# Optimization experiments

Hardware: AMD Instinct MI355X
Metric: run time of the kernel (lower is better)

Reference implementation:

```python
import jax, jax.numpy as jnp
import numpy as np

TOP_K = 4
NORM_TOPK_PROB = False  # Qwen2-MoE default

def setup_inputs() -> dict:
    key = jax.random.key(0)
    ks = jax.random.split(key, 10)
    B, S, D = 1, 2048, 2048
    E, F, FS = 8, 1408, 5632
    s = 0.02
    return {
        "hidden_states": jax.random.normal(ks[0], (B, S, D), jnp.float32),
        "gate_w": jax.random.normal(ks[1], (E, D), jnp.float32) * s,          # router Linear weight [E, D]
        "Wg": jax.random.normal(ks[2], (E, D, F), jnp.float32) * s,           # expert gate_proj
        "Wu": jax.random.normal(ks[3], (E, D, F), jnp.float32) * s,           # expert up_proj
        "Wd": jax.random.normal(ks[4], (E, F, D), jnp.float32) * s,           # expert down_proj
        "Wsg": jax.random.normal(ks[5], (D, FS), jnp.float32) * s,            # shared gate_proj
        "Wsu": jax.random.normal(ks[6], (D, FS), jnp.float32) * s,            # shared up_proj
        "Wsd": jax.random.normal(ks[7], (FS, D), jnp.float32) * s,            # shared down_proj
        "shared_gate_w": jax.random.normal(ks[8], (D, 1), jnp.float32) * s,   # shared_expert_gate Linear(D,1)
    }

def reference(hidden_states, gate_w, Wg, Wu, Wd, Wsg, Wsu, Wsd, shared_gate_w):
    B, S, D = hidden_states.shape
    x = hidden_states.reshape(-1, D)                       # [T, D]
    T = x.shape[0]
    router_logits = x @ gate_w.T                           # [T, E]
    probs = jax.nn.softmax(router_logits.astype(jnp.float32), axis=-1)
    top_vals, top_idx = jax.lax.top_k(probs, TOP_K)        # [T, K]
    if NORM_TOPK_PROB:
        top_vals = top_vals / jnp.sum(top_vals, axis=-1, keepdims=True)
    # dense routing-weight matrix: zero for unselected experts (same math as masked naive loop)
    w = jnp.zeros_like(probs).at[jnp.arange(T)[:, None], top_idx].set(top_vals)
    w = w.astype(x.dtype)                                  # [T, E]
    # per-expert SiLU-gated MLP, computed densely over all experts
    h = jax.nn.silu(jnp.einsum('td,edf->etf', x, Wg)) * jnp.einsum('td,edf->etf', x, Wu)  # [E, T, F]
    expert_out = jnp.einsum('etf,efd->etd', h, Wd)         # [E, T, D]
    moe_out = jnp.einsum('etd,te->td', expert_out, w)      # [T, D]
    # shared expert with sigmoid gate
    shared = (jax.nn.silu(x @ Wsg) * (x @ Wsu)) @ Wsd      # [T, D]
    shared = jax.nn.sigmoid(x @ shared_gate_w) * shared    # [T,1] * [T,D]
    out = (moe_out + shared).reshape(B, S, D)
    return out, router_logits
```

## Files before the change

kernel.cpp:

```cpp
#include <hip/hip_runtime.h>
#include <hip/hip_bf16.h>

typedef __attribute__((ext_vector_type(8))) __bf16 bf16x8;
typedef __attribute__((ext_vector_type(4))) float f32x4;

#define TKN 2048
#define DMODEL 2048
#define NEXP 8
#define FEXP 1408
#define FSH 5632

__device__ __forceinline__ unsigned short f2bf(float f) {
  unsigned u = __float_as_uint(f);
  u += 0x7FFFu + ((u >> 16) & 1u);
  return (unsigned short)(u >> 16);
}
__device__ __forceinline__ unsigned pk2(float a, float b) {
  return (unsigned)f2bf(a) | ((unsigned)f2bf(b) << 16);
}

__device__ __forceinline__ void gll16(const void* g, void* l) {
  __builtin_amdgcn_global_load_lds(
      (const __attribute__((address_space(1))) unsigned*)g,
      (__attribute__((address_space(3))) unsigned*)l, 16, 0, 0);
}

enum { EPI_GU = 0, EPI_DOWN = 1, EPI_SDOWN = 2 };

__global__ __launch_bounds__(256)
void router_k(const float* __restrict__ x, const float* __restrict__ gw,
              const float* __restrict__ sgw, float* __restrict__ logits,
              float* __restrict__ sig, int* __restrict__ cnt,
              int* __restrict__ tokl, float* __restrict__ wls)
{
  const int wv = threadIdx.x >> 6, lane = threadIdx.x & 63;
  const int t = blockIdx.x * 4 + wv;
  const float* xr = x + (long)t * DMODEL;
  float xv[32];
#pragma unroll
  for (int j = 0; j < 32; j++) xv[j] = xr[lane + (j << 6)];

  float lg[8];
#pragma unroll
  for (int e = 0; e < 8; e++) {
    const float* gr = gw + (long)e * DMODEL;
    float acc = 0.f;
#pragma unroll
    for (int j = 0; j < 32; j++) acc += xv[j] * gr[lane + (j << 6)];
#pragma unroll
    for (int s = 1; s < 64; s <<= 1) acc += __shfl_xor(acc, s, 64);
    lg[e] = acc;
  }
  float sgacc = 0.f;
#pragma unroll
  for (int j = 0; j < 32; j++) sgacc += xv[j] * sgw[lane + (j << 6)];
#pragma unroll
  for (int s = 1; s < 64; s <<= 1) sgacc += __shfl_xor(sgacc, s, 64);

  if (lane == 0) {
    float mx = lg[0];
#pragma unroll
    for (int e = 1; e < 8; e++) mx = fmaxf(mx, lg[e]);
    float p[8], se = 0.f;
#pragma unroll
    for (int e = 0; e < 8; e++) { p[e] = expf(lg[e] - mx); se += p[e]; }
    float inv = 1.f / se;
#pragma unroll
    for (int e = 0; e < 8; e++) { p[e] *= inv; logits[t * 8 + e] = lg[e]; }
    sig[t] = 1.f / (1.f + expf(-sgacc));
#pragma unroll
    for (int k = 0; k < 4; k++) {
      int bi = 0; float bv = p[0];
#pragma unroll
      for (int e = 1; e < 8; e++) if (p[e] > bv) { bv = p[e]; bi = e; }
      p[bi] = -1.f;
      int pos = atomicAdd(&cnt[bi], 1);
      tokl[bi * TKN + pos] = t;
      wls[bi * TKN + pos] = bv;
    }
  }
}

__global__ void scan_k(const int* __restrict__ cnt, int* __restrict__ offs) {
  if (threadIdx.x == 0) {
    int s = 0;
    for (int e = 0; e < 8; e++) { offs[e] = s; s += cnt[e]; }
    offs[8] = s;
  }
}

__global__ __launch_bounds__(256)
void cvt_x_k(const float* __restrict__ x, char* __restrict__ xbf)
{
  long id = (long)blockIdx.x * 256 + threadIdx.x;
  int row = id >> 8, u = id & 255, kt = u >> 2, j = u & 3;
  const float* p = x + (long)row * 2048 + kt * 32 + j * 4;
  float4 a = *(const float4*)p;
  float4 b = *(const float4*)(p + 16);
  uint4 o;
  o.x = pk2(a.x, a.y); o.y = pk2(a.z, a.w);
  o.z = pk2(b.x, b.y); o.w = pk2(b.z, b.w);
  *(uint4*)(xbf + id * 16) = o;
}

__global__ __launch_bounds__(256)
void cvt_w_k(const float* __restrict__ W, long sB, int N,
             char* __restrict__ panel, long panStride)
{
  const int ct = blockIdx.x, kt = blockIdx.y, e = blockIdx.z, KT = gridDim.y;
  const float* Wp = W + (long)e * sB + (long)(kt * 32) * N + ct * 128;
  __shared__ float t[32][128];
  const int r = threadIdx.x >> 3, q = threadIdx.x & 7;
  const float* rp = Wp + (long)r * N + q * 16;
  float4 f0 = *(const float4*)(rp + 0);
  float4 f1 = *(const float4*)(rp + 4);
  float4 f2 = *(const float4*)(rp + 8);
  float4 f3 = *(const float4*)(rp + 12);
  *(float4*)&t[r][q * 16 + 0]  = f0;
  *(float4*)&t[r][q * 16 + 4]  = f1;
  *(float4*)&t[r][q * 16 + 8]  = f2;
  *(float4*)&t[r][q * 16 + 12] = f3;
  __syncthreads();
  char* outp = panel + e * panStride + ((long)ct * KT + kt) * 8192;
#pragma unroll
  for (int uu = 0; uu < 2; uu++) {
    int u = threadIdx.x + uu * 256;
    int c = u >> 2;
    int g = (u & 3) ^ ((c >> 1) & 3);
    uint4 o;
    o.x = pk2(t[g * 4 + 0][c], t[g * 4 + 1][c]);
    o.y = pk2(t[g * 4 + 2][c], t[g * 4 + 3][c]);
    o.z = pk2(t[16 + g * 4 + 0][c], t[16 + g * 4 + 1][c]);
    o.w = pk2(t[16 + g * 4 + 2][c], t[16 + g * 4 + 3][c]);
    *(uint4*)(outp + u * 16) = o;
  }
}

template<int EPI, bool EXPERT, int KSPLIT>
__global__ __launch_bounds__(256, 2)
void gemm2_k(const char* __restrict__ Abf, long strA,
             const char* __restrict__ Bp, const char* __restrict__ Bp2,
             long sBpan, int KTtot, int NCT,
             void* __restrict__ O, int ldKo,
             const int* __restrict__ cnt, const int* __restrict__ offs,
             const int* __restrict__ tokl, const float* __restrict__ wls,
             const float* __restrict__ sig)
{
  constexpr bool FUSED = (EPI == EPI_GU);
  const int tid = threadIdx.x, lane = tid & 63, w = tid >> 6;
  const int wg = blockIdx.x;

  int e = 0, rt, ct, kc = 0, M = TKN;
  if (EXPERT) {
    e = wg & 7; int q = wg >> 3; rt = q & 15; ct = q >> 4;
    M = cnt[e];
    if (rt * 128 >= M) return;
  } else {
    rt = wg & 15; int q = wg >> 4; ct = q % NCT; kc = q / NCT;
  }
  const int KT = KTtot / KSPLIT;
  const int kt0 = kc * KT;
  const int obase = EXPERT ? offs[e] : 0;

  __shared__ int s_tok[128];
  __shared__ float s_w[128];
  __shared__ alignas(16) char Ab[3][8192];
  __shared__ alignas(16) char Bb[3][8192];
  __shared__ alignas(16) char Bb2[FUSED ? 3 : 1][FUSED ? 8192 : 16];

  if (EXPERT) {
    if (tid < 128) {
      int r = rt * 128 + tid;
      int rc = (r < M) ? r : (M - 1);
      s_tok[tid] = tokl[e * TKN + rc];
      if (EPI == EPI_DOWN) s_w[tid] = (r < M) ? wls[e * TKN + r] : 0.f;
    }
    __syncthreads();
  }

  const int lrow0 = w * 32 + (lane >> 2);
  const int lrow1 = lrow0 + 16;
  auto rowbyte = [&](int rl) -> long {
    long gr;
    if (EPI == EPI_DOWN) { int r = rt * 128 + rl; gr = obase + ((r < M) ? r : (M - 1)); }
    else if (EXPERT)     { gr = s_tok[rl]; }
    else                 { gr = rt * 128 + rl; }
    return gr * strA;
  };
  const int au0 = (lane & 3) ^ ((lrow0 >> 1) & 3);
  const int au1 = (lane & 3) ^ ((lrow1 >> 1) & 3);
  const char* gA0 = Abf + rowbyte(lrow0) + (long)kt0 * 64 + au0 * 16;
  const char* gA1 = Abf + rowbyte(lrow1) + (long)kt0 * 64 + au1 * 16;
  const long bbase = (EXPERT ? (long)e * sBpan : 0) + ((long)ct * KTtot + kt0) * 8192
                     + w * 2048 + (long)lane * 16;
  const char* gB  = Bp + bbase;
  const char* gB2 = FUSED ? (Bp2 + bbase) : nullptr;

  auto stage = [&](int bf, int kt) {
    long ao = (long)kt * 64, bo = (long)kt * 8192;
    gll16(gA0 + ao, &Ab[bf][w * 2048]);
    gll16(gA1 + ao, &Ab[bf][w * 2048 + 1024]);
    gll16(gB + bo, &Bb[bf][w * 2048]);
    gll16(gB + bo + 1024, &Bb[bf][w * 2048 + 1024]);
    if constexpr (FUSED) {
      gll16(gB2 + bo, &Bb2[bf][w * 2048]);
      gll16(gB2 + bo + 1024, &Bb2[bf][w * 2048 + 1024]);
    }
  };

  const int wm = w >> 1, wn = w & 1, g = lane >> 4, l15 = lane & 15;
  int raOff[4], rbOff[4];
#pragma unroll
  for (int m = 0; m < 4; m++) {
    int row = wm * 64 + m * 16 + l15;
    raOff[m] = row * 64 + ((g ^ ((row >> 1) & 3)) << 4);
  }
#pragma unroll
  for (int n = 0; n < 4; n++) {
    int col = wn * 64 + n * 16 + l15;
    rbOff[n] = col * 64 + ((g ^ ((col >> 1) & 3)) << 4);
  }

  f32x4 acc[4][4] = {};
  f32x4 acc2[4][4] = {};

  stage(0, 0);
  stage(1, 1);

  int rd = 0;
#pragma unroll 1
  for (int kt = 0; kt < KT; ++kt) {
    if (kt + 1 < KT) {
      if constexpr (FUSED) asm volatile("s_waitcnt vmcnt(6)" ::: "memory");
      else                 asm volatile("s_waitcnt vmcnt(4)" ::: "memory");
    } else {
      asm volatile("s_waitcnt vmcnt(0)" ::: "memory");
    }
    __builtin_amdgcn_s_barrier();
    __builtin_amdgcn_sched_barrier(0);

    bf16x8 av[4], bg[4], bu[4];
#pragma unroll
    for (int m = 0; m < 4; m++) av[m] = *(const bf16x8*)&Ab[rd][raOff[m]];
#pragma unroll
    for (int n = 0; n < 4; n++) {
      bg[n] = *(const bf16x8*)&Bb[rd][rbOff[n]];
      if constexpr (FUSED) bu[n] = *(const bf16x8*)&Bb2[rd][rbOff[n]];
    }

    int wr = rd + 2; if (wr >= 3) wr -= 3;
    if (kt + 2 < KT) stage(wr, kt + 2);

    __builtin_amdgcn_s_setprio(1);
#pragma unroll
    for (int m = 0; m < 4; m++)
#pragma unroll
      for (int n = 0; n < 4; n++) {
        acc[m][n] = __builtin_amdgcn_mfma_f32_16x16x32_bf16(av[m], bg[n], acc[m][n], 0, 0, 0);
        if constexpr (FUSED)
          acc2[m][n] = __builtin_amdgcn_mfma_f32_16x16x32_bf16(av[m], bu[n], acc2[m][n], 0, 0, 0);
      }
    __builtin_amdgcn_s_setprio(0);
    __builtin_amdgcn_sched_barrier(0);
    rd = (rd == 2) ? 0 : rd + 1;
  }

#pragma unroll
  for (int m = 0; m < 4; m++) {
#pragma unroll
    for (int n = 0; n < 4; n++) {
      int col = ct * 128 + wn * 64 + n * 16 + l15;
      f32x4 a = acc[m][n];
      f32x4 a2 = acc2[m][n];
#pragma unroll
      for (int q = 0; q < 4; q++) {
        int rl = wm * 64 + m * 16 + (g << 2) + q;
        int grow = rt * 128 + rl;
        float v = a[q];
        if constexpr (EPI == EPI_GU) {
          if (!EXPERT || grow < M) {
            float hv = (v / (1.f + __expf(-v))) * a2[q];
            long byteoff = (long)(obase + grow) * ((long)ldKo * 64)
                         + (col >> 5) * 64 + ((col >> 2) & 3) * 16
                         + ((col & 16) >> 1) + (col & 3) * 2;
            *(unsigned short*)((char*)O + byteoff) = f2bf(hv);
          }
        } else if constexpr (EPI == EPI_DOWN) {
          if (grow < M)
            atomicAdd((float*)O + (long)s_tok[rl] * DMODEL + col, s_w[rl] * v);
        } else {
          atomicAdd((float*)O + (long)grow * DMODEL + col, sig[grow] * v);
        }
      }
    }
  }
}

__device__ __forceinline__ void block_sync_fb() {
  __builtin_amdgcn_sched_barrier(0);
  asm volatile("s_waitcnt lgkmcnt(0)" ::: "memory");
  __builtin_amdgcn_s_barrier();
  __builtin_amdgcn_sched_barrier(0);
}

template<int EPI, bool EXPERT, int KSPLIT>
__global__ __launch_bounds__(256, 2)
void gemm_fb_k(const float* __restrict__ A, int lda,
               const float* __restrict__ B, const float* __restrict__ B2,
               long sB, int ldb, int Ktot,
               float* __restrict__ O, int ldo,
               const int* __restrict__ cnt, const int* __restrict__ offs,
               const int* __restrict__ tokl, const float* __restrict__ wls,
               const float* __restrict__ sig)
{
  constexpr bool FUSED = (EPI == EPI_GU);
  const int tid = threadIdx.x;
  const int lane = tid & 63;

  int e = 0, rt, kc = 0, M = TKN;
  if (EXPERT) {
    e = blockIdx.y >> 4; rt = blockIdx.y & 15;
    M = cnt[e];
    if (rt * 128 >= M) return;
  } else {
    rt = blockIdx.y & 15; kc = blockIdx.y >> 4;
  }
  const int K = Ktot / KSPLIT;
  const int koff = kc * K;
  const int colblk = blockIdx.x * 128;
  const float* Bp  = B + (EXPERT ? (long)e * sB : 0);
  const float* Bp2 = FUSED ? (B2 + (EXPERT ? (long)e * sB : 0)) : nullptr;
  const int obase = EXPERT ? offs[e] : 0;

  __shared__ alignas(16) unsigned char Ab[8192];
  __shared__ alignas(16) unsigned char Bb[8192];
  __shared__ alignas(16) unsigned char Bb2[FUSED ? 8192 : 16];
  __shared__ int s_tok[128];
  __shared__ float s_w[128];

  if (EXPERT && tid < 128) {
    int r = rt * 128 + tid;
    int rc = (r < M) ? r : (M - 1);
    s_tok[tid] = tokl[e * TKN + rc];
    if (EPI == EPI_DOWN) s_w[tid] = (r < M) ? wls[e * TKN + r] : 0.f;
  }
  if (EXPERT) __syncthreads();

  const int arowl = tid >> 1;
  const int ahalf = tid & 1;
  long arow;
  if (EPI == EPI_DOWN) {
    int r = rt * 128 + arowl;
    arow = (long)obase + ((r < M) ? r : (M - 1));
  } else if (EXPERT) {
    arow = s_tok[arowl];
  } else {
    arow = rt * 128 + arowl;
  }
  const float* aptr = A + arow * (long)lda + koff + ahalf * 16;
  int wa[4];
#pragma unroll
  for (int j = 0; j < 4; j++)
    wa[j] = arowl * 64 + ((j ^ ((arowl ^ (arowl >> 3)) & 3)) << 4) + ahalf * 8;

  const int kg = tid >> 5, ng = tid & 31;
  const float* bptr  = Bp + (long)(koff + kg * 4) * ldb + colblk + ng * 4;
  const float* bptr2 = FUSED ? (Bp2 + (long)(koff + kg * 4) * ldb + colblk + ng * 4) : nullptr;
  int wb[4];
#pragma unroll
  for (int i = 0; i < 4; i++) {
    int c = ng * 4 + i;
    wb[i] = c * 64 + ((((kg & 3) ^ ((c ^ (c >> 3)) & 3))) << 4) + (kg >> 2) * 8;
  }

  const int wid = tid >> 6, wm = wid >> 1, wn = wid & 1;
  const int g = lane >> 4, l15 = lane & 15;
  int ra[4], rb[4];
#pragma unroll
  for (int m = 0; m < 4; m++) {
    int r = wm * 64 + m * 16 + l15;
    ra[m] = r * 64 + ((g ^ ((r ^ (r >> 3)) & 3)) << 4);
  }
#pragma unroll
  for (int n = 0; n < 4; n++) {
    int c = wn * 64 + n * 16 + l15;
    rb[n] = c * 64 + ((g ^ ((c ^ (c >> 3)) & 3)) << 4);
  }

  f32x4 acc[4][4] = {};
  f32x4 acc2[4][4] = {};

  const int KT = K >> 5;
  float4 ta0[4], tb0[4], tc0[4], ta1[4], tb1[4], tc1[4];

  auto load_tile = [&](float4* ra_, float4* rb_, float4* rc_, int kt) {
    const float4* a4 = reinterpret_cast<const float4*>(aptr + kt * 32);
    ra_[0] = a4[0]; ra_[1] = a4[1]; ra_[2] = a4[2]; ra_[3] = a4[3];
    const float* bb = bptr + (long)kt * 32 * ldb;
    rb_[0] = *reinterpret_cast<const float4*>(bb);
    rb_[1] = *reinterpret_cast<const float4*>(bb + ldb);
    rb_[2] = *reinterpret_cast<const float4*>(bb + 2 * ldb);
    rb_[3] = *reinterpret_cast<const float4*>(bb + 3 * ldb);
    if (FUSED) {
      const float* cc = bptr2 + (long)kt * 32 * ldb;
      rc_[0] = *reinterpret_cast<const float4*>(cc);
      rc_[1] = *reinterpret_cast<const float4*>(cc + ldb);
      rc_[2] = *reinterpret_cast<const float4*>(cc + 2 * ldb);
      rc_[3] = *reinterpret_cast<const float4*>(cc + 3 * ldb);
    }
  };

  auto store_tile = [&](const float4* ra_, const float4* rb_, const float4* rc_) {
#pragma unroll
    for (int j = 0; j < 4; j++)
      *reinterpret_cast<uint2*>(Ab + wa[j]) =
          make_uint2(pk2(ra_[j].x, ra_[j].y), pk2(ra_[j].z, ra_[j].w));
    *reinterpret_cast<uint2*>(Bb + wb[0]) = make_uint2(pk2(rb_[0].x, rb_[1].x), pk2(rb_[2].x, rb_[3].x));
    *reinterpret_cast<uint2*>(Bb + wb[1]) = make_uint2(pk2(rb_[0].y, rb_[1].y), pk2(rb_[2].y, rb_[3].y));
    *reinterpret_cast<uint2*>(Bb + wb[2]) = make_uint2(pk2(rb_[0].z, rb_[1].z), pk2(rb_[2].z, rb_[3].z));
    *reinterpret_cast<uint2*>(Bb + wb[3]) = make_uint2(pk2(rb_[0].w, rb_[1].w), pk2(rb_[2].w, rb_[3].w));
    if (FUSED) {
      *reinterpret_cast<uint2*>(Bb2 + wb[0]) = make_uint2(pk2(rc_[0].x, rc_[1].x), pk2(rc_[2].x, rc_[3].x));
      *reinterpret_cast<uint2*>(Bb2 + wb[1]) = make_uint2(pk2(rc_[0].y, rc_[1].y), pk2(rc_[2].y, rc_[3].y));
      *reinterpret_cast<uint2*>(Bb2 + wb[2]) = make_uint2(pk2(rc_[0].z, rc_[1].z), pk2(rc_[2].z, rc_[3].z));
      *reinterpret_cast<uint2*>(Bb2 + wb[3]) = make_uint2(pk2(rc_[0].w, rc_[1].w), pk2(rc_[2].w, rc_[3].w));
    }
  };

  auto mfma_step = [&]() {
    bf16x8 av[4], bvg[4], bvu[4];
#pragma unroll
    for (int m = 0; m < 4; m++) av[m] = *reinterpret_cast<const bf16x8*>(Ab + ra[m]);
#pragma unroll
    for (int n = 0; n < 4; n++) {
      bvg[n] = *reinterpret_cast<const bf16x8*>(Bb + rb[n]);
      if (FUSED) bvu[n] = *reinterpret_cast<const bf16x8*>(Bb2 + rb[n]);
    }
#pragma unroll
    for (int m = 0; m < 4; m++)
#pragma unroll
      for (int n = 0; n < 4; n++) {
        acc[m][n] = __builtin_amdgcn_mfma_f32_16x16x32_bf16(av[m], bvg[n], acc[m][n], 0, 0, 0);
        if (FUSED)
          acc2[m][n] = __builtin_amdgcn_mfma_f32_16x16x32_bf16(av[m], bvu[n], acc2[m][n], 0, 0, 0);
      }
  };

  load_tile(ta0, tb0, tc0, 0);
#pragma unroll 1
  for (int kt = 0; kt < KT; kt += 2) {
    load_tile(ta1, tb1, tc1, kt + 1);
    store_tile(ta0, tb0, tc0);
    block_sync_fb();
    mfma_step();
    block_sync_fb();
    int k2 = (kt + 2 < KT) ? kt + 2 : 0;
    load_tile(ta0, tb0, tc0, k2);
    store_tile(ta1, tb1, tc1);
    block_sync_fb();
    mfma_step();
    block_sync_fb();
  }

#pragma unroll
  for (int m = 0; m < 4; m++) {
#pragma unroll
    for (int n = 0; n < 4; n++) {
      int col = colblk + wn * 64 + n * 16 + l15;
      f32x4 a = acc[m][n];
      f32x4 a2 = acc2[m][n];
#pragma unroll
      for (int q = 0; q < 4; q++) {
        int rl = wm * 64 + m * 16 + (g << 2) + q;
        int grow = rt * 128 + rl;
        float v = a[q];
        if (EPI == EPI_GU) {
          if (!EXPERT || grow < M) {
            float hv = (v / (1.f + __expf(-v))) * a2[q];
            O[(long)(obase + grow) * ldo + col] = hv;
          }
        } else if (EPI == EPI_DOWN) {
          if (grow < M)
            atomicAdd(&O[(long)s_tok[rl] * ldo + col], s_w[rl] * v);
        } else {
          atomicAdd(&O[(long)grow * ldo + col], sig[grow] * v);
        }
      }
    }
  }
}

extern "C" void kernel_launch(void* const* d_in, const int* in_sizes, int n_in,
                              void* d_out, int out_size, void* d_ws, size_t ws_size,
                              hipStream_t stream)
{
  (void)in_sizes; (void)n_in; (void)out_size;
  const float* x   = (const float*)d_in[0];
  const float* gw  = (const float*)d_in[1];
  const float* Wg  = (const float*)d_in[2];
  const float* Wu  = (const float*)d_in[3];
  const float* Wd  = (const float*)d_in[4];
  const float* Wsg = (const float*)d_in[5];
  const float* Wsu = (const float*)d_in[6];
  const float* Wsd = (const float*)d_in[7];
  const float* sgw = (const float*)d_in[8];

  float* out    = (float*)d_out;
  float* logits = out + (long)TKN * DMODEL;

  char* w    = (char*)d_ws;
  int*  cnt  = (int*)w;
  int*  offs = (int*)(w + 64);
  float* sig = (float*)(w + 1024);
  int*  tokl = (int*)(w + 16384);
  float* wls = (float*)(w + 81920);

  hipMemsetAsync(out, 0, (size_t)TKN * DMODEL * 4, stream);
  hipMemsetAsync(cnt, 0, 64, stream);

  router_k<<<dim3(TKN / 4), 256, 0, stream>>>(x, gw, sgw, logits, sig, cnt, tokl, wls);
  scan_k<<<1, 64, 0, stream>>>(cnt, offs);

  const size_t NEED = 241172480ull;
  if (ws_size >= NEED) {
    char* xbf   = w + 262144;
    char* h     = w + 8650752;
    char* pan   = w + 33554432;
    char* panWg  = pan;
    char* panWu  = pan + 46137344;
    char* panWd  = pan + 92274688;
    char* panWsg = pan + 138412032;
    char* panWsu = pan + 161480704;
    char* panWsd = pan + 184549376;
    const long sPan = 5767168;

    cvt_x_k<<<dim3(2048), 256, 0, stream>>>(x, xbf);
    cvt_w_k<<<dim3(11, 64, 8), 256, 0, stream>>>(Wg, (long)DMODEL * FEXP, FEXP, panWg, sPan);
    cvt_w_k<<<dim3(11, 64, 8), 256, 0, stream>>>(Wu, (long)DMODEL * FEXP, FEXP, panWu, sPan);
    cvt_w_k<<<dim3(16, 44, 8), 256, 0, stream>>>(Wd, (long)FEXP * DMODEL, DMODEL, panWd, sPan);
    cvt_w_k<<<dim3(44, 64, 1), 256, 0, stream>>>(Wsg, 0, FSH, panWsg, 0);
    cvt_w_k<<<dim3(44, 64, 1), 256, 0, stream>>>(Wsu, 0, FSH, panWsu, 0);
    cvt_w_k<<<dim3(16, 176, 1), 256, 0, stream>>>(Wsd, 0, DMODEL, panWsd, 0);

    gemm2_k<EPI_GU, true, 1><<<dim3(8 * 16 * 11), 256, 0, stream>>>(
        xbf, 4096, panWg, panWu, sPan, 64, 11, h, 44, cnt, offs, tokl, wls, nullptr);
    gemm2_k<EPI_DOWN, true, 1><<<dim3(8 * 16 * 16), 256, 0, stream>>>(
        h, 2816, panWd, nullptr, sPan, 44, 16, out, 0, cnt, offs, tokl, wls, nullptr);
    gemm2_k<EPI_GU, false, 1><<<dim3(16 * 44), 256, 0, stream>>>(
        xbf, 4096, panWsg, panWsu, 0, 64, 44, h, 176, nullptr, nullptr, nullptr, nullptr, nullptr);
    gemm2_k<EPI_SDOWN, false, 4><<<dim3(16 * 16 * 4), 256, 0, stream>>>(
        h, 11264, panWsd, nullptr, 0, 176, 16, out, 0, nullptr, nullptr, nullptr, nullptr, sig);
  } else {
    float* h = (float*)(w + (1 << 20));
    gemm_fb_k<EPI_GU, true, 1><<<dim3(FEXP / 128, 128), 256, 0, stream>>>(
        x, DMODEL, Wg, Wu, (long)DMODEL * FEXP, FEXP, DMODEL, h, FEXP, cnt, offs, tokl, wls, nullptr);
    gemm_fb_k<EPI_DOWN, true, 1><<<dim3(DMODEL / 128, 128), 256, 0, stream>>>(
        h, FEXP, Wd, nullptr, (long)FEXP * DMODEL, DMODEL, FEXP, out, DMODEL, cnt, offs, tokl, wls, nullptr);
    gemm_fb_k<EPI_GU, false, 1><<<dim3(FSH / 128, TKN / 128), 256, 0, stream>>>(
        x, DMODEL, Wsg, Wsu, 0, FSH, DMODEL, h, FSH, nullptr, nullptr, nullptr, nullptr, nullptr);
    gemm_fb_k<EPI_SDOWN, false, 4><<<dim3(DMODEL / 128, (TKN / 128) * 4), 256, 0, stream>>>(
        h, FSH, Wsd, nullptr, 0, DMODEL, FSH, out, DMODEL, nullptr, nullptr, nullptr, nullptr, sig);
  }
}
```

Before: 691.1 us.

## Interleave gate/up weight panels so fused GU GEMM uses single B stream

A new conversion kernel interleaves the gate and up projection weights into one bf16 panel: each 128-column tile holds 64 gate columns and the matching 64 up columns. The gate/up GEMM then loads a single B tile and keeps a single accumulator set, and its epilogue pairs acc[n] with acc[n+2] to apply SiLU*up. This halves LDS and register use per block (possibly allowing higher occupancy) and merges two conversion launches into one. In exchange it launches twice as many GU blocks, each producing only 64 output columns, so A tiles are reloaded more often.

After: 679.8 us, median of 4. About the same (-1.6%).

```diff
diff --git a/kernel.cpp b/kernel.cpp
--- a/kernel.cpp
+++ b/kernel.cpp
@@ -136,17 +136,49 @@
   }
 }
 
+__global__ __launch_bounds__(256)
+void cvt_gu_k(const float* __restrict__ Wg, const float* __restrict__ Wu,
+              long sB, int N, char* __restrict__ panel, long panStride)
+{
+  const int ct = blockIdx.x, kt = blockIdx.y, e = blockIdx.z, KT = gridDim.y;
+  __shared__ float t[32][128];
+  const int r = threadIdx.x >> 3, q = threadIdx.x & 7;
+  const float* src = ((q >> 1) & 1) ? Wu : Wg;
+  const int scol = ct * 64 + ((q >> 2) << 5) + ((q & 1) << 4);
+  const float* rp = src + (long)e * sB + (long)(kt * 32 + r) * N + scol;
+  float4 f0 = *(const float4*)(rp + 0);
+  float4 f1 = *(const float4*)(rp + 4);
+  float4 f2 = *(const float4*)(rp + 8);
+  float4 f3 = *(const float4*)(rp + 12);
+  *(float4*)&t[r][q * 16 + 0]  = f0;
+  *(float4*)&t[r][q * 16 + 4]  = f1;
+  *(float4*)&t[r][q * 16 + 8]  = f2;
+  *(float4*)&t[r][q * 16 + 12] = f3;
+  __syncthreads();
+  char* outp = panel + e * panStride + ((long)ct * KT + kt) * 8192;
+#pragma unroll
+  for (int uu = 0; uu < 2; uu++) {
+    int u = threadIdx.x + uu * 256;
+    int c = u >> 2;
+    int g = (u & 3) ^ ((c >> 1) & 3);
+    uint4 o;
+    o.x = pk2(t[g * 4 + 0][c], t[g * 4 + 1][c]);
+    o.y = pk2(t[g * 4 + 2][c], t[g * 4 + 3][c]);
+    o.z = pk2(t[16 + g * 4 + 0][c], t[16 + g * 4 + 1][c]);
+    o.w = pk2(t[16 + g * 4 + 2][c], t[16 + g * 4 + 3][c]);
+    *(uint4*)(outp + u * 16) = o;
+  }
+}
+
 template<int EPI, bool EXPERT, int KSPLIT>
 __global__ __launch_bounds__(256, 2)
 void gemm2_k(const char* __restrict__ Abf, long strA,
-             const char* __restrict__ Bp, const char* __restrict__ Bp2,
-             long sBpan, int KTtot, int NCT,
+             const char* __restrict__ Bp, long sBpan, int KTtot, int NCT,
              void* __restrict__ O, int ldKo,
              const int* __restrict__ cnt, const int* __restrict__ offs,
              const int* __restrict__ tokl, const float* __restrict__ wls,
              const float* __restrict__ sig)
 {
-  constexpr bool FUSED = (EPI == EPI_GU);
   const int tid = threadIdx.x, lane = tid & 63, w = tid >> 6;
   const int wg = blockIdx.x;
 
@@ -166,7 +198,6 @@
   __shared__ float s_w[128];
   __shared__ alignas(16) char Ab[3][8192];
   __shared__ alignas(16) char Bb[3][8192];
-  __shared__ alignas(16) char Bb2[FUSED ? 3 : 1][FUSED ? 8192 : 16];
 
   if (EXPERT) {
     if (tid < 128) {
@@ -193,8 +224,7 @@
   const char* gA1 = Abf + rowbyte(lrow1) + (long)kt0 * 64 + au1 * 16;
   const long bbase = (EXPERT ? (long)e * sBpan : 0) + ((long)ct * KTtot + kt0) * 8192
                      + w * 2048 + (long)lane * 16;
-  const char* gB  = Bp + bbase;
-  const char* gB2 = FUSED ? (Bp2 + bbase) : nullptr;
+  const char* gB = Bp + bbase;
 
   auto stage = [&](int bf, int kt) {
     long ao = (long)kt * 64, bo = (long)kt * 8192;
@@ -202,10 +232,6 @@
     gll16(gA1 + ao, &Ab[bf][w * 2048 + 1024]);
     gll16(gB + bo, &Bb[bf][w * 2048]);
     gll16(gB + bo + 1024, &Bb[bf][w * 2048 + 1024]);
-    if constexpr (FUSED) {
-      gll16(gB2 + bo, &Bb2[bf][w * 2048]);
-      gll16(gB2 + bo + 1024, &Bb2[bf][w * 2048 + 1024]);
-    }
   };
 
   const int wm = w >> 1, wn = w & 1, g = lane >> 4, l15 = lane & 15;
@@ -222,7 +248,6 @@
   }
 
   f32x4 acc[4][4] = {};
-  f32x4 acc2[4][4] = {};
 
   stage(0, 0);
   stage(1, 1);
@@ -230,23 +255,16 @@
   int rd = 0;
 #pragma unroll 1
   for (int kt = 0; kt < KT; ++kt) {
-    if (kt + 1 < KT) {
-      if constexpr (FUSED) asm volatile("s_waitcnt vmcnt(6)" ::: "memory");
-      else                 asm volatile("s_waitcnt vmcnt(4)" ::: "memory");
-    } else {
-      asm volatile("s_waitcnt vmcnt(0)" ::: "memory");
-    }
+    if (kt + 1 < KT) asm volatile("s_waitcnt vmcnt(4)" ::: "memory");
+    else             asm volatile("s_waitcnt vmcnt(0)" ::: "memory");
     __builtin_amdgcn_s_barrier();
     __builtin_amdgcn_sched_barrier(0);
 
-    bf16x8 av[4], bg[4], bu[4];
+    bf16x8 av[4], bv[4];
 #pragma unroll
     for (int m = 0; m < 4; m++) av[m] = *(const bf16x8*)&Ab[rd][raOff[m]];
 #pragma unroll
-    for (int n = 0; n < 4; n++) {
-      bg[n] = *(const bf16x8*)&Bb[rd][rbOff[n]];
-      if constexpr (FUSED) bu[n] = *(const bf16x8*)&Bb2[rd][rbOff[n]];
-    }
+    for (int n = 0; n < 4; n++) bv[n] = *(const bf16x8*)&Bb[rd][rbOff[n]];
 
     int wr = rd + 2; if (wr >= 3) wr -= 3;
     if (kt + 2 < KT) stage(wr, kt + 2);
@@ -255,41 +273,54 @@
 #pragma unroll
     for (int m = 0; m < 4; m++)
 #pragma unroll
-      for (int n = 0; n < 4; n++) {
-        acc[m][n] = __builtin_amdgcn_mfma_f32_16x16x32_bf16(av[m], bg[n], acc[m][n], 0, 0, 0);
-        if constexpr (FUSED)
-          acc2[m][n] = __builtin_amdgcn_mfma_f32_16x16x32_bf16(av[m], bu[n], acc2[m][n], 0, 0, 0);
-      }
+      for (int n = 0; n < 4; n++)
+        acc[m][n] = __builtin_amdgcn_mfma_f32_16x16x32_bf16(av[m], bv[n], acc[m][n], 0, 0, 0);
     __builtin_amdgcn_s_setprio(0);
     __builtin_amdgcn_sched_barrier(0);
     rd = (rd == 2) ? 0 : rd + 1;
   }
 
-#pragma unroll
-  for (int m = 0; m < 4; m++) {
-#pragma unroll
-    for (int n = 0; n < 4; n++) {
-      int col = ct * 128 + wn * 64 + n * 16 + l15;
-      f32x4 a = acc[m][n];
-      f32x4 a2 = acc2[m][n];
-#pragma unroll
-      for (int q = 0; q < 4; q++) {
-        int rl = wm * 64 + m * 16 + (g << 2) + q;
-        int grow = rt * 128 + rl;
-        float v = a[q];
-        if constexpr (EPI == EPI_GU) {
+  if constexpr (EPI == EPI_GU) {
+#pragma unroll
+    for (int m = 0; m < 4; m++) {
+#pragma unroll
+      for (int n = 0; n < 2; n++) {
+        int lc = ct * 64 + wn * 32 + n * 16 + l15;
+        f32x4 ga = acc[m][n];
+        f32x4 ua = acc[m][n + 2];
+#pragma unroll
+        for (int q = 0; q < 4; q++) {
+          int rl = wm * 64 + m * 16 + (g << 2) + q;
+          int grow = rt * 128 + rl;
           if (!EXPERT || grow < M) {
-            float hv = (v / (1.f + __expf(-v))) * a2[q];
+            float gv = ga[q];
+            float hv = (gv / (1.f + __expf(-gv))) * ua[q];
             long byteoff = (long)(obase + grow) * ((long)ldKo * 64)
-                         + (col >> 5) * 64 + ((col >> 2) & 3) * 16
-                         + ((col & 16) >> 1) + (col & 3) * 2;
+                         + (lc >> 5) * 64 + ((lc >> 2) & 3) * 16
+                         + ((lc & 16) >> 1) + (lc & 3) * 2;
             *(unsigned short*)((char*)O + byteoff) = f2bf(hv);
           }
-        } else if constexpr (EPI == EPI_DOWN) {
-          if (grow < M)
-            atomicAdd((float*)O + (long)s_tok[rl] * DMODEL + col, s_w[rl] * v);
-        } else {
-          atomicAdd((float*)O + (long)grow * DMODEL + col, sig[grow] * v);
+        }
+      }
+    }
+  } else {
+#pragma unroll
+    for (int m = 0; m < 4; m++) {
+#pragma unroll
+      for (int n = 0; n < 4; n++) {
+        int col = ct * 128 + wn * 64 + n * 16 + l15;
+        f32x4 a = acc[m][n];
+#pragma unroll
+        for (int q = 0; q < 4; q++) {
+          int rl = wm * 64 + m * 16 + (g << 2) + q;
+          int grow = rt * 128 + rl;
+          float v = a[q];
+          if constexpr (EPI == EPI_DOWN) {
+            if (grow < M)
+              atomicAdd((float*)O + (long)s_tok[rl] * DMODEL + col, s_w[rl] * v);
+          } else {
+            atomicAdd((float*)O + (long)grow * DMODEL + col, sig[grow] * v);
+          }
         }
       }
     }
@@ -523,33 +554,29 @@
 
   const size_t NEED = 241172480ull;
   if (ws_size >= NEED) {
-    char* xbf   = w + 262144;
-    char* h     = w + 8650752;
-    char* pan   = w + 33554432;
-    char* panWg  = pan;
-    char* panWu  = pan + 46137344;
-    char* panWd  = pan + 92274688;
-    char* panWsg = pan + 138412032;
-    char* panWsu = pan + 161480704;
-    char* panWsd = pan + 184549376;
-    const long sPan = 5767168;
+    char* xbf     = w + 262144;
+    char* h       = w + 8650752;
+    char* panGUex = w + 33554432;
+    char* panWd   = w + 125829120;
+    char* panGUsh = w + 171966464;
+    char* panWsd  = w + 218103808;
+    const long sPanGU = 11534336;
+    const long sPanWd = 5767168;
 
     cvt_x_k<<<dim3(2048), 256, 0, stream>>>(x, xbf);
-    cvt_w_k<<<dim3(11, 64, 8), 256, 0, stream>>>(Wg, (long)DMODEL * FEXP, FEXP, panWg, sPan);
-    cvt_w_k<<<dim3(11, 64, 8), 256, 0, stream>>>(Wu, (long)DMODEL * FEXP, FEXP, panWu, sPan);
-    cvt_w_k<<<dim3(16, 44, 8), 256, 0, stream>>>(Wd, (long)FEXP * DMODEL, DMODEL, panWd, sPan);
-    cvt_w_k<<<dim3(44, 64, 1), 256, 0, stream>>>(Wsg, 0, FSH, panWsg, 0);
-    cvt_w_k<<<dim3(44, 64, 1), 256, 0, stream>>>(Wsu, 0, FSH, panWsu, 0);
+    cvt_gu_k<<<dim3(22, 64, 8), 256, 0, stream>>>(Wg, Wu, (long)DMODEL * FEXP, FEXP, panGUex, sPanGU);
+    cvt_w_k<<<dim3(16, 44, 8), 256, 0, stream>>>(Wd, (long)FEXP * DMODEL, DMODEL, panWd, sPanWd);
+    cvt_gu_k<<<dim3(88, 64, 1), 256, 0, stream>>>(Wsg, Wsu, 0, FSH, panGUsh, 0);
     cvt_w_k<<<dim3(16, 176, 1), 256, 0, stream>>>(Wsd, 0, DMODEL, panWsd, 0);
 
-    gemm2_k<EPI_GU, true, 1><<<dim3(8 * 16 * 11), 256, 0, stream>>>(
-        xbf, 4096, panWg, panWu, sPan, 64, 11, h, 44, cnt, offs, tokl, wls, nullptr);
+    gemm2_k<EPI_GU, true, 1><<<dim3(8 * 16 * 22), 256, 0, stream>>>(
+        xbf, 4096, panGUex, sPanGU, 64, 22, h, 44, cnt, offs, tokl, wls, nullptr);
     gemm2_k<EPI_DOWN, true, 1><<<dim3(8 * 16 * 16), 256, 0, stream>>>(
-        h, 2816, panWd, nullptr, sPan, 44, 16, out, 0, cnt, offs, tokl, wls, nullptr);
-    gemm2_k<EPI_GU, false, 1><<<dim3(16 * 44), 256, 0, stream>>>(
-        xbf, 4096, panWsg, panWsu, 0, 64, 44, h, 176, nullptr, nullptr, nullptr, nullptr, nullptr);
+        h, 2816, panWd, sPanWd, 44, 16, out, 0, cnt, offs, tokl, wls, nullptr);
+    gemm2_k<EPI_GU, false, 1><<<dim3(16 * 88), 256, 0, stream>>>(
+        xbf, 4096, panGUsh, 0, 64, 88, h, 176, nullptr, nullptr, nullptr, nullptr, nullptr);
     gemm2_k<EPI_SDOWN, false, 4><<<dim3(16 * 16 * 4), 256, 0, stream>>>(
-        h, 11264, panWsd, nullptr, 0, 176, 16, out, 0, nullptr, nullptr, nullptr, nullptr, sig);
+        h, 11264, panWsd, 0, 176, 16, out, 0, nullptr, nullptr, nullptr, nullptr, sig);
   } else {
     float* h = (float*)(w + (1 << 20));
     gemm_fb_k<EPI_GU, true, 1><<<dim3(FEXP / 128, 128), 256, 0, stream>>>(
```
